# Kernel tuning notes

Hardware: AMD Instinct MI355X
Metric: run time of the kernel (lower is better)

## Reference

```python
import jax, jax.numpy as jnp
import numpy as np

D = 512          # input_dim == hidden size of MinLSTM layers
OUT = 1          # output_dim of fc_out
B, T = 8, 4096
LN_EPS = 1e-5


def _linear_params(key, d_in, d_out):
    kw, kb = jax.random.split(key)
    lim = 1.0 / np.sqrt(d_in)
    W = jax.random.uniform(kw, (d_out, d_in), minval=-lim, maxval=lim, dtype=jnp.float32)
    b = jax.random.uniform(kb, (d_out,), minval=-lim, maxval=lim, dtype=jnp.float32)
    return W, b


def setup_inputs() -> dict:
    key = jax.random.key(0)
    ks = jax.random.split(key, 8)
    x = jax.random.normal(ks[0], (B, T, D), dtype=jnp.float32)
    Wf0, bf0 = _linear_params(ks[1], D, D)
    Wi0, bi0 = _linear_params(ks[2], D, D)
    Wh0, bh0 = _linear_params(ks[3], D, D)
    Wf1, bf1 = _linear_params(ks[4], D, D)
    Wi1, bi1 = _linear_params(ks[5], D, D)
    Wh1, bh1 = _linear_params(ks[6], D, D)
    W_out, b_out = _linear_params(ks[7], D, OUT)
    ln_g = jnp.ones((D,), dtype=jnp.float32)
    ln_b = jnp.zeros((D,), dtype=jnp.float32)
    return {
        'x': x,
        'Wf0': Wf0, 'bf0': bf0, 'Wi0': Wi0, 'bi0': bi0, 'Wh0': Wh0, 'bh0': bh0,
        'Wf1': Wf1, 'bf1': bf1, 'Wi1': Wi1, 'bi1': bi1, 'Wh1': Wh1, 'bh1': bh1,
        'ln_g': ln_g, 'ln_b': ln_b, 'W_out': W_out, 'b_out': b_out,
    }


def _minlstm(x, Wf, bf, Wi, bi, Wh, bh):
    # minLSTM (parallel form, h0 = 0):
    #   f = sigma(W_f x), i = sigma(W_i x), h~ = W_h x
    #   f' = f/(f+i), i' = i/(f+i)
    #   h_t = f'_t * h_{t-1} + i'_t * h~_t   (linear recurrence -> associative scan)
    f = jax.nn.sigmoid(jnp.einsum('btd,ed->bte', x, Wf) + bf)
    i = jax.nn.sigmoid(jnp.einsum('btd,ed->bte', x, Wi) + bi)
    h_tilde = jnp.einsum('btd,ed->bte', x, Wh) + bh
    denom = f + i
    a = f / denom                      # decay coefficient f'
    u = (i / denom) * h_tilde          # input contribution i' * h~

    def combine(c1, c2):
        a1, u1 = c1
        a2, u2 = c2
        return a1 * a2, a2 * u1 + u2

    _, h = jax.lax.associative_scan(combine, (a, u), axis=1)
    return h  # [B, T, D]


def reference(x, Wf0, bf0, Wi0, bi0, Wh0, bh0,
              Wf1, bf1, Wi1, bi1, Wh1, bh1,
              ln_g, ln_b, W_out, b_out):
    h = _minlstm(x, Wf0, bf0, Wi0, bi0, Wh0, bh0)
    h = _minlstm(h, Wf1, bf1, Wi1, bi1, Wh1, bh1)
    h = jnp.where(jnp.isnan(h), x, h)      # NaN fallback to input
    h = x + h                               # residual
    # LayerNorm over last dim
    mu = jnp.mean(h, axis=-1, keepdims=True)
    var = jnp.mean(jnp.square(h - mu), axis=-1, keepdims=True)
    hn = (h - mu) * jax.lax.rsqrt(var + LN_EPS) * ln_g + ln_b
    # output projection [B, T, OUT]
    return jnp.einsum('btd,od->bto', hn, W_out) + b_out
```

## Files before the change

### kernel.cpp

```cpp
#include <hip/hip_runtime.h>
#include <hip/hip_bf16.h>
#include <stdint.h>


#define MROWS 32768
#define DDIM  512
#define TLEN  4096
#define BSZ   8
#define NCHUNK 64
#define CLEN   64

typedef __attribute__((ext_vector_type(8))) __bf16 bf16x8;
typedef __attribute__((ext_vector_type(16))) float f32x16;
typedef __attribute__((ext_vector_type(4))) unsigned short ushort4_t;

static __device__ __forceinline__ unsigned short f2bf(float f) {
    unsigned int u = __float_as_uint(f);
    u = (u + 0x7FFFu + ((u >> 16) & 1u)) >> 16;
    return (unsigned short)u;
}
static __device__ __forceinline__ float bf2f(unsigned short s) {
    return __uint_as_float(((unsigned int)s) << 16);
}
static __device__ __forceinline__ void gload_lds16(const void* gptr, void* ldsp) {
    __builtin_amdgcn_global_load_lds(
        (const __attribute__((address_space(1))) uint32_t*)gptr,
        (__attribute__((address_space(3))) uint32_t*)ldsp,
        16, 0, 0);
}

#define WAITV(n) asm volatile("s_waitcnt vmcnt(" #n ")" ::: "memory")

__global__ __launch_bounds__(256) void cast_all(
    const float4* __restrict__ x,
    const float4* __restrict__ w0, const float4* __restrict__ w1,
    const float4* __restrict__ w2, const float4* __restrict__ w3,
    const float4* __restrict__ w4, const float4* __restrict__ w5,
    ushort4_t* __restrict__ xb, ushort4_t* __restrict__ wb)
{
    int i = blockIdx.x * 256 + threadIdx.x;
    float4 v;
    ushort4_t* dst;
    if (i < 4194304) {
        v = x[i];
        dst = xb + i;
    } else {
        int j = i - 4194304;
        int wsel = j >> 16;
        int rem = j & 65535;
        const float4* src = (wsel == 0) ? w0 : (wsel == 1) ? w1 : (wsel == 2) ? w2
                          : (wsel == 3) ? w3 : (wsel == 4) ? w4 : w5;
        v = src[rem];
        dst = wb + j;
    }
    ushort4_t o;
    o.x = f2bf(v.x); o.y = f2bf(v.y); o.z = f2bf(v.z); o.w = f2bf(v.w);
    *dst = o;
}

__global__ __launch_bounds__(256, 3) void gates_gemm(
    const unsigned short* __restrict__ X,
    const unsigned short* __restrict__ Wf,
    const unsigned short* __restrict__ Wi,
    const unsigned short* __restrict__ Wh,
    const float* __restrict__ bf_, const float* __restrict__ bi_,
    const float* __restrict__ bh_,
    unsigned int* __restrict__ au_out,
    float* __restrict__ Asum, float* __restrict__ Usum)
{
    __shared__ __align__(16) unsigned short lds[2 * 10240];

    const int tid  = threadIdx.x;
    const int lane = tid & 63;
    const int wave = tid >> 6;
    const int wm = wave >> 1;
    const int wn = wave & 1;
    const int ln31 = lane & 31;
    const int kh = lane >> 5;

    const int w = blockIdx.x;
    const int xcd = w & 7;
    const int s = w >> 3;
    const int by = xcd * 32 + (s >> 3);
    const int bx = s & 7;
    const int mblk = by * 128;
    const int nblk = bx * 64;

    const int srow = tid >> 2;
    const int c4   = tid & 3;
    const int cg   = ((c4 ^ ((srow >> 1) & 3)) << 3);
    const int tid8 = tid * 8;
    const unsigned short* g0 = X  + (size_t)(mblk + srow) * 512 + cg;
    const unsigned short* g1 = X  + (size_t)(mblk + 64 + srow) * 512 + cg;
    const unsigned short* g2 = Wf + (size_t)(nblk + srow) * 512 + cg;
    const unsigned short* g3 = Wi + (size_t)(nblk + srow) * 512 + cg;
    const unsigned short* g4 = Wh + (size_t)(nblk + srow) * 512 + cg;

    int aoff[2][2], boff[2];
#pragma unroll
    for (int mi = 0; mi < 2; ++mi) {
        int row = wm * 64 + mi * 32 + ln31;
#pragma unroll
        for (int ks = 0; ks < 2; ++ks)
            aoff[mi][ks] = row * 32 + (((2 * ks + kh) ^ ((row >> 1) & 3)) << 3);
    }
    {
        int brow = wn * 32 + ln31;
#pragma unroll
        for (int ks = 0; ks < 2; ++ks)
            boff[ks] = brow * 32 + (((2 * ks + kh) ^ ((brow >> 1) & 3)) << 3);
    }

    f32x16 accF[2], accI[2], accH[2];
#pragma unroll
    for (int mi = 0; mi < 2; ++mi) {
#pragma unroll
        for (int e = 0; e < 16; ++e) { accF[mi][e] = 0.f; accI[mi][e] = 0.f; accH[mi][e] = 0.f; }
    }

#define STAGE(bb) do { \
    gload_lds16(g0, lds + (bb) + tid8);            \
    gload_lds16(g1, lds + (bb) + 2048 + tid8);     \
    gload_lds16(g2, lds + (bb) + 4096 + tid8);     \
    gload_lds16(g3, lds + (bb) + 6144 + tid8);     \
    gload_lds16(g4, lds + (bb) + 8192 + tid8);     \
    g0 += 32; g1 += 32; g2 += 32; g3 += 32; g4 += 32; } while (0)

    STAGE(0);

#pragma unroll
    for (int t = 0; t < 16; ++t) {
        if (t < 15) {
            STAGE(((t + 1) & 1) * 10240);
            WAITV(5);
        } else {
            WAITV(0);
        }
        __builtin_amdgcn_s_barrier();
        __builtin_amdgcn_sched_barrier(0);

        const unsigned short* cb = lds + (t & 1) * 10240;
#pragma unroll
        for (int ks = 0; ks < 2; ++ks) {
            bf16x8 af[2];
            af[0] = *reinterpret_cast<const bf16x8*>(cb + aoff[0][ks]);
            af[1] = *reinterpret_cast<const bf16x8*>(cb + aoff[1][ks]);
            bf16x8 bF = *reinterpret_cast<const bf16x8*>(cb + 4096 + boff[ks]);
            bf16x8 bI = *reinterpret_cast<const bf16x8*>(cb + 6144 + boff[ks]);
            bf16x8 bH = *reinterpret_cast<const bf16x8*>(cb + 8192 + boff[ks]);
            __builtin_amdgcn_s_setprio(1);
#pragma unroll
            for (int mi = 0; mi < 2; ++mi) {
                accF[mi] = __builtin_amdgcn_mfma_f32_32x32x16_bf16(af[mi], bF, accF[mi], 0, 0, 0);
                accI[mi] = __builtin_amdgcn_mfma_f32_32x32x16_bf16(af[mi], bI, accI[mi], 0, 0, 0);
                accH[mi] = __builtin_amdgcn_mfma_f32_32x32x16_bf16(af[mi], bH, accH[mi], 0, 0, 0);
            }
            __builtin_amdgcn_s_setprio(0);
        }
        __builtin_amdgcn_sched_barrier(0);
        __builtin_amdgcn_s_barrier();
        __builtin_amdgcn_sched_barrier(0);
    }
#undef STAGE

    const int n = nblk + wn * 32 + ln31;
    const float bfv = bf_[n], biv = bi_[n], bhv = bh_[n];
    const bool up = (lane & 32) != 0;
    float ca = 1.f, cu = 0.f;
#pragma unroll
    for (int mi = 0; mi < 2; ++mi) {
#pragma unroll
        for (int j = 0; j < 4; ++j) {
            float sa = 1.f, su = 0.f;
#pragma unroll
            for (int r = 0; r < 4; ++r) {
                const int reg = 4 * j + r;
                const int m = mblk + wm * 64 + mi * 32 + 8 * j + 4 * kh + r;
                float zf = accF[mi][reg] + bfv;
                float zi = accI[mi][reg] + biv;
                float zh = accH[mi][reg] + bhv;
                float ef = __expf(-zf);
                float ei = __expf(-zi);
                float inv = __frcp_rn(2.0f + ef + ei);
                float av = (1.0f + ei) * inv;
                float uv = (1.0f + ef) * inv * zh;
                au_out[(size_t)m * 512 + n] =
                    ((unsigned int)f2bf(uv) << 16) | (unsigned int)f2bf(av);
                su = av * su + uv; sa *= av;
            }
            float oa = __shfl_xor(sa, 32), ou = __shfl_xor(su, 32);
            float ta = sa * oa;
            float tu = up ? (sa * ou + su) : (oa * su + ou);
            cu = ta * cu + tu; ca = ca * ta;
        }
    }
    if (lane < 32) {
        size_t ci = (size_t)(by * 2 + wm) * 512 + n;
        Asum[ci] = ca;
        Usum[ci] = cu;
    }
}

__global__ void scan_pass2(const float4* __restrict__ Asum, const float4* __restrict__ Usum,
                           float4* __restrict__ Hinit) {
    int t = blockIdx.x * 256 + threadIdx.x;
    int d4 = t & 127;
    int b = t >> 7;
    float4 h = {0.f, 0.f, 0.f, 0.f};
    for (int c = 0; c < NCHUNK; ++c) {
        size_t idx = (size_t)(b * NCHUNK + c) * 128 + d4;
        Hinit[idx] = h;
        float4 A = Asum[idx]; float4 U = Usum[idx];
        h.x = A.x * h.x + U.x; h.y = A.y * h.y + U.y;
        h.z = A.z * h.z + U.z; h.w = A.w * h.w + U.w;
    }
}

__global__ void scan_pass3(const uint4* __restrict__ au,
                           const float4* __restrict__ Hinit,
                           ushort4_t* __restrict__ hout) {
    int gid = blockIdx.x * 256 + threadIdx.x;
    int d4 = gid & 127;
    int c  = (gid >> 7) & 63;
    int b  = gid >> 13;
    size_t base = (size_t)(b * TLEN + c * CLEN) * 128 + d4;
    size_t s4 = (size_t)(b * NCHUNK + c) * 128 + d4;
    float4 h0 = Hinit[s4];
    float h[4] = {h0.x, h0.y, h0.z, h0.w};
#pragma unroll 4
    for (int l = 0; l < CLEN; ++l) {
        size_t idx = base + (size_t)l * 128;
        uint4 v = au[idx];
        unsigned int vv[4] = {v.x, v.y, v.z, v.w};
        ushort4_t o;
#pragma unroll
        for (int j = 0; j < 4; ++j) {
            float av = __uint_as_float(vv[j] << 16);
            float uv = __uint_as_float(vv[j] & 0xFFFF0000u);
            h[j] = av * h[j] + uv;
            o[j] = f2bf(h[j]);
        }
        hout[idx] = o;
    }
}

__global__ __launch_bounds__(128) void scan3_final(
    const uint4* __restrict__ au, const float4* __restrict__ Hinit,
    const float4* __restrict__ x4,
    const float* __restrict__ g, const float* __restrict__ bvec,
    const float* __restrict__ Wout, const float* __restrict__ bout,
    float* __restrict__ out)
{
    const int blk = blockIdx.x;
    const int b = blk >> 6, c = blk & 63;
    const int d4 = threadIdx.x;
    const int lane = threadIdx.x & 63;
    const int wv = threadIdx.x >> 6;

    float4 h0 = Hinit[(size_t)blk * 128 + d4];
    float h[4] = {h0.x, h0.y, h0.z, h0.w};
    float4 g4 = reinterpret_cast<const float4*>(g)[d4];
    float4 b4 = reinterpret_cast<const float4*>(bvec)[d4];
    float4 w4 = reinterpret_cast<const float4*>(Wout)[d4];
    const float ga[4] = {g4.x, g4.y, g4.z, g4.w};
    const float ba[4] = {b4.x, b4.y, b4.z, b4.w};
    const float wa[4] = {w4.x, w4.y, w4.z, w4.w};
    const float bo = bout[0];

    __shared__ float redS[2], redQ[2], redP[2];
    size_t base = ((size_t)b * TLEN + c * CLEN) * 128 + d4;

    for (int l = 0; l < CLEN; ++l) {
        size_t idx = base + (size_t)l * 128;
        uint4 v = au[idx];
        float4 xr = x4[idx];
        const unsigned int vv[4] = {v.x, v.y, v.z, v.w};
        const float xa[4] = {xr.x, xr.y, xr.z, xr.w};
        float r[4];
        float sfl = 0.f, q = 0.f;
#pragma unroll
        for (int j = 0; j < 4; ++j) {
            float av = __uint_as_float(vv[j] << 16);
            float uv = __uint_as_float(vv[j] & 0xFFFF0000u);
            h[j] = av * h[j] + uv;
            float hv = h[j];
            if (hv != hv) hv = xa[j];
            float rr = xa[j] + hv;
            r[j] = rr;
            sfl += rr; q += rr * rr;
        }
#pragma unroll
        for (int m = 32; m >= 1; m >>= 1) {
            sfl += __shfl_xor(sfl, m);
            q += __shfl_xor(q, m);
        }
        if (lane == 0) { redS[wv] = sfl; redQ[wv] = q; }
        __syncthreads();
        float st = redS[0] + redS[1];
        float qt = redQ[0] + redQ[1];
        float mu = st * (1.0f / 512.0f);
        float var = qt * (1.0f / 512.0f) - mu * mu;
        float rstd = rsqrtf(var + 1e-5f);
        float p = 0.f;
#pragma unroll
        for (int j = 0; j < 4; ++j)
            p += ((r[j] - mu) * rstd * ga[j] + ba[j]) * wa[j];
#pragma unroll
        for (int m = 32; m >= 1; m >>= 1) p += __shfl_xor(p, m);
        if (lane == 0) redP[wv] = p;
        __syncthreads();
        if (threadIdx.x == 0)
            out[(size_t)b * TLEN + c * CLEN + l] = redP[0] + redP[1] + bo;
    }
}

extern "C" void kernel_launch(void* const* d_in, const int* in_sizes, int n_in,
                              void* d_out, int out_size, void* d_ws, size_t ws_size,
                              hipStream_t stream) {
    const float* x    = (const float*)d_in[0];
    const float* Wf0  = (const float*)d_in[1];  const float* bf0 = (const float*)d_in[2];
    const float* Wi0  = (const float*)d_in[3];  const float* bi0 = (const float*)d_in[4];
    const float* Wh0  = (const float*)d_in[5];  const float* bh0 = (const float*)d_in[6];
    const float* Wf1  = (const float*)d_in[7];  const float* bf1 = (const float*)d_in[8];
    const float* Wi1  = (const float*)d_in[9];  const float* bi1 = (const float*)d_in[10];
    const float* Wh1  = (const float*)d_in[11]; const float* bh1 = (const float*)d_in[12];
    const float* ln_g = (const float*)d_in[13]; const float* ln_b = (const float*)d_in[14];
    const float* W_out = (const float*)d_in[15]; const float* b_out = (const float*)d_in[16];

    char* ws = (char*)d_ws;
    unsigned short* Xb = (unsigned short*)ws;  ws += (size_t)MROWS * DDIM * 2;
    unsigned short* Wball = (unsigned short*)ws;
    unsigned short* Wb[6];
    for (int i = 0; i < 6; ++i) { Wb[i] = (unsigned short*)ws; ws += (size_t)DDIM * DDIM * 2; }
    unsigned int* aubuf = (unsigned int*)ws; ws += (size_t)MROWS * DDIM * 4;
    float* Asum = (float*)ws;  ws += (size_t)BSZ * NCHUNK * DDIM * 4;
    float* Usum = (float*)ws;  ws += (size_t)BSZ * NCHUNK * DDIM * 4;
    float* Hinit = (float*)ws; ws += (size_t)BSZ * NCHUNK * DDIM * 4;
    unsigned short* h0b = (unsigned short*)ws; ws += (size_t)MROWS * DDIM * 2;

    cast_all<<<17920, 256, 0, stream>>>(
        (const float4*)x, (const float4*)Wf0, (const float4*)Wi0, (const float4*)Wh0,
        (const float4*)Wf1, (const float4*)Wi1, (const float4*)Wh1,
        (ushort4_t*)Xb, (ushort4_t*)Wball);

    gates_gemm<<<2048, 256, 0, stream>>>(Xb, Wb[0], Wb[1], Wb[2], bf0, bi0, bh0,
                                         aubuf, Asum, Usum);
    scan_pass2<<<4, 256, 0, stream>>>((const float4*)Asum, (const float4*)Usum, (float4*)Hinit);
    scan_pass3<<<256, 256, 0, stream>>>((const uint4*)aubuf, (const float4*)Hinit, (ushort4_t*)h0b);

    gates_gemm<<<2048, 256, 0, stream>>>(h0b, Wb[3], Wb[4], Wb[5], bf1, bi1, bh1,
                                         aubuf, Asum, Usum);
    scan_pass2<<<4, 256, 0, stream>>>((const float4*)Asum, (const float4*)Usum, (float4*)Hinit);
    scan3_final<<<512, 128, 0, stream>>>((const uint4*)aubuf, (const float4*)Hinit,
                                         (const float4*)x, ln_g, ln_b, W_out, b_out,
                                         (float*)d_out);
}
```

Before: 246.2 us.

## Triple-buffer gates GEMM LDS pipeline and change swizzle to cut bank conflicts

Moves the gates GEMM from double to triple LDS buffering. Two stages are prefetched up front and the next load is issued right after the barrier, which lets the trailing barrier in each iteration go. The XOR swizzle now also mixes in row bit 3 to reduce LDS bank conflicts, and the loads and MFMAs are reordered so the first MFMA can start sooner. The larger LDS footprint lowers the occupancy hint from 3 to 2 blocks per CU.

```diff
diff --git a/kernel.cpp b/kernel.cpp
--- a/kernel.cpp
+++ b/kernel.cpp
@@ -58,7 +58,7 @@
     *dst = o;
 }
 
-__global__ __launch_bounds__(256, 3) void gates_gemm(
+__global__ __launch_bounds__(256, 2) void gates_gemm(
     const unsigned short* __restrict__ X,
     const unsigned short* __restrict__ Wf,
     const unsigned short* __restrict__ Wi,
@@ -68,7 +68,7 @@
     unsigned int* __restrict__ au_out,
     float* __restrict__ Asum, float* __restrict__ Usum)
 {
-    __shared__ __align__(16) unsigned short lds[2 * 10240];
+    __shared__ __align__(16) unsigned short lds[3 * 10240];
 
     const int tid  = threadIdx.x;
     const int lane = tid & 63;
@@ -88,7 +88,7 @@
 
     const int srow = tid >> 2;
     const int c4   = tid & 3;
-    const int cg   = ((c4 ^ ((srow >> 1) & 3)) << 3);
+    const int cg   = ((c4 ^ (((srow >> 1) ^ (srow >> 3)) & 3)) << 3);
     const int tid8 = tid * 8;
     const unsigned short* g0 = X  + (size_t)(mblk + srow) * 512 + cg;
     const unsigned short* g1 = X  + (size_t)(mblk + 64 + srow) * 512 + cg;
@@ -96,19 +96,20 @@
     const unsigned short* g3 = Wi + (size_t)(nblk + srow) * 512 + cg;
     const unsigned short* g4 = Wh + (size_t)(nblk + srow) * 512 + cg;
 
+    const int fl = ((ln31 >> 1) ^ (ln31 >> 3)) & 3;
     int aoff[2][2], boff[2];
 #pragma unroll
     for (int mi = 0; mi < 2; ++mi) {
         int row = wm * 64 + mi * 32 + ln31;
 #pragma unroll
         for (int ks = 0; ks < 2; ++ks)
-            aoff[mi][ks] = row * 32 + (((2 * ks + kh) ^ ((row >> 1) & 3)) << 3);
+            aoff[mi][ks] = row * 32 + (((2 * ks + kh) ^ fl) << 3);
     }
     {
         int brow = wn * 32 + ln31;
 #pragma unroll
         for (int ks = 0; ks < 2; ++ks)
-            boff[ks] = brow * 32 + (((2 * ks + kh) ^ ((brow >> 1) & 3)) << 3);
+            boff[ks] = brow * 32 + (((2 * ks + kh) ^ fl) << 3);
     }
 
     f32x16 accF[2], accI[2], accH[2];
@@ -127,38 +128,34 @@
     g0 += 32; g1 += 32; g2 += 32; g3 += 32; g4 += 32; } while (0)
 
     STAGE(0);
+    STAGE(10240);
 
 #pragma unroll
     for (int t = 0; t < 16; ++t) {
-        if (t < 15) {
-            STAGE(((t + 1) & 1) * 10240);
-            WAITV(5);
-        } else {
-            WAITV(0);
-        }
+        if (t < 15) { WAITV(5); }
+        else        { WAITV(0); }
         __builtin_amdgcn_s_barrier();
         __builtin_amdgcn_sched_barrier(0);
 
-        const unsigned short* cb = lds + (t & 1) * 10240;
+        if (t < 14) STAGE(((t + 2) % 3) * 10240);
+
+        const unsigned short* cb = lds + (t % 3) * 10240;
 #pragma unroll
         for (int ks = 0; ks < 2; ++ks) {
-            bf16x8 af[2];
-            af[0] = *reinterpret_cast<const bf16x8*>(cb + aoff[0][ks]);
-            af[1] = *reinterpret_cast<const bf16x8*>(cb + aoff[1][ks]);
-            bf16x8 bF = *reinterpret_cast<const bf16x8*>(cb + 4096 + boff[ks]);
-            bf16x8 bI = *reinterpret_cast<const bf16x8*>(cb + 6144 + boff[ks]);
-            bf16x8 bH = *reinterpret_cast<const bf16x8*>(cb + 8192 + boff[ks]);
+            bf16x8 af0 = *reinterpret_cast<const bf16x8*>(cb + aoff[0][ks]);
+            bf16x8 bF  = *reinterpret_cast<const bf16x8*>(cb + 4096 + boff[ks]);
+            bf16x8 af1 = *reinterpret_cast<const bf16x8*>(cb + aoff[1][ks]);
+            bf16x8 bI  = *reinterpret_cast<const bf16x8*>(cb + 6144 + boff[ks]);
+            bf16x8 bH  = *reinterpret_cast<const bf16x8*>(cb + 8192 + boff[ks]);
             __builtin_amdgcn_s_setprio(1);
-#pragma unroll
-            for (int mi = 0; mi < 2; ++mi) {
-                accF[mi] = __builtin_amdgcn_mfma_f32_32x32x16_bf16(af[mi], bF, accF[mi], 0, 0, 0);
-                accI[mi] = __builtin_amdgcn_mfma_f32_32x32x16_bf16(af[mi], bI, accI[mi], 0, 0, 0);
-                accH[mi] = __builtin_amdgcn_mfma_f32_32x32x16_bf16(af[mi], bH, accH[mi], 0, 0, 0);
-            }
+            accF[0] = __builtin_amdgcn_mfma_f32_32x32x16_bf16(af0, bF, accF[0], 0, 0, 0);
+            accF[1] = __builtin_amdgcn_mfma_f32_32x32x16_bf16(af1, bF, accF[1], 0, 0, 0);
+            accI[0] = __builtin_amdgcn_mfma_f32_32x32x16_bf16(af0, bI, accI[0], 0, 0, 0);
+            accI[1] = __builtin_amdgcn_mfma_f32_32x32x16_bf16(af1, bI, accI[1], 0, 0, 0);
+            accH[0] = __builtin_amdgcn_mfma_f32_32x32x16_bf16(af0, bH, accH[0], 0, 0, 0);
+            accH[1] = __builtin_amdgcn_mfma_f32_32x32x16_bf16(af1, bH, accH[1], 0, 0, 0);
             __builtin_amdgcn_s_setprio(0);
         }
-        __builtin_amdgcn_sched_barrier(0);
-        __builtin_amdgcn_s_barrier();
         __builtin_amdgcn_sched_barrier(0);
     }
 #undef STAGE
```

Result: no change. 246.6 us (+0.2%).
